# Kernel optimization log

Measured on AMD Instinct MI355X. Metric: run time of the kernel, lower is better.

The kernel has to match this reference:

```python
import jax, jax.numpy as jnp
import numpy as np

D_MODEL = 2048
NUM_HEADS = 32
HEAD_DIM = D_MODEL // NUM_HEADS  # 64
ROPE_BASE = 10000.0


def _rope_cos_sin(seq_len, head_dim, dtype):
    inv_freq = 1.0 / (ROPE_BASE ** (jnp.arange(0, head_dim, 2, dtype=jnp.float32) / head_dim))
    freqs = jnp.arange(seq_len, dtype=jnp.float32)[:, None] * inv_freq[None, :]  # (S, Dh/2)
    emb = jnp.concatenate([freqs, freqs], axis=-1)  # (S, Dh)
    return emb.astype(dtype), jnp.cos(emb).astype(dtype), jnp.sin(emb).astype(dtype)


def _rotate_half(x):
    x1, x2 = jnp.split(x, 2, axis=-1)
    return jnp.concatenate([-x2, x1], axis=-1)


def setup_inputs() -> dict:
    key = jax.random.key(0)
    k1, k2, k3, k4 = jax.random.split(key, 4)
    B, S, D = 1, 2048, D_MODEL
    x = jax.random.normal(k1, (B, S, D), dtype=jnp.float32)
    Wqkv = jax.random.normal(k2, (3 * D, D), dtype=jnp.float32) * 0.02
    Wo = jax.random.normal(k3, (D, D), dtype=jnp.float32) * 0.02
    gate = jax.random.normal(k4, (D,), dtype=jnp.float32) * 0.1
    return {"x": x, "Wqkv": Wqkv, "Wo": Wo, "gate": gate}


def reference(x, Wqkv, Wo, gate):
    B, S, D = x.shape
    H, Dh = NUM_HEADS, HEAD_DIM
    residual = x

    # fused QKV projection (torch Linear: y = x @ W.T)
    qkv = jnp.einsum('bsd,ed->bse', x, Wqkv).reshape(B, S, 3, H, Dh)
    q, k, v = qkv[:, :, 0], qkv[:, :, 1], qkv[:, :, 2]  # each (B, S, H, Dh)

    # RoPE
    _, cos, sin = _rope_cos_sin(S, Dh, x.dtype)
    cos = cos[None, :, None, :]  # (1, S, 1, Dh)
    sin = sin[None, :, None, :]
    q = q * cos + _rotate_half(q) * sin
    k = k * cos + _rotate_half(k) * sin

    # causal SDPA
    scale = 1.0 / np.sqrt(Dh)
    scores = jnp.einsum('bqhd,bkhd->bhqk', q, k) * scale  # (B, H, S, S)
    causal = jnp.tril(jnp.ones((S, S), dtype=bool))
    scores = jnp.where(causal[None, None], scores, jnp.finfo(scores.dtype).min)
    probs = jax.nn.softmax(scores, axis=-1)
    attn = jnp.einsum('bhqk,bkhd->bqhd', probs, v).reshape(B, S, D)

    out = jnp.einsum('bsd,ed->bse', attn, Wo)
    # HeoGate: learned per-channel gated residual (assumption; see notes)
    return residual + gate * out
```

## Files before the change

kernel.cpp:

```cpp
#include <hip/hip_runtime.h>
#include <hip/hip_bf16.h>
#include <cstdint>
#include <cstddef>

typedef __hip_bfloat16 bf16;
typedef short short8 __attribute__((ext_vector_type(8)));
typedef float f32x4 __attribute__((ext_vector_type(4)));

#define S_LEN 2048
#define DMODEL 2048
#define NQKV 6144
#define NHEADS 32
#define HDIM 64
#define ROPE_L2 0.4152410118609203f
#define Q_PRESCALE 0.18033688011112042f

__device__ __forceinline__ void async_copy16(const bf16* g, bf16* l) {
  __builtin_amdgcn_global_load_lds(
      (const __attribute__((address_space(1))) void*)g,
      (__attribute__((address_space(3))) void*)l, 16, 0, 0);
}

__device__ __forceinline__ f32x4 mfma_bf16(short8 a, short8 b, f32x4 c) {
  return __builtin_amdgcn_mfma_f32_16x16x32_bf16(a, b, c, 0, 0, 0);
}

__global__ __launch_bounds__(256) void cvt3_kernel(const float* __restrict__ sx,
                                                   bf16* __restrict__ dx,
                                                   const float* __restrict__ sw,
                                                   bf16* __restrict__ dw,
                                                   const float* __restrict__ so,
                                                   bf16* __restrict__ dov) {
  int i = blockIdx.x * 256 + threadIdx.x;
  const float* s;
  bf16* d;
  if (i < 1048576) {
    s = sx; d = dx;
  } else if (i < 4194304) {
    s = sw; d = dw; i -= 1048576;
  } else {
    s = so; d = dov; i -= 4194304;
  }
  const float4 v = ((const float4*)s)[i];
  union { bf16 h[4]; ushort4 u; } tmp;
  tmp.h[0] = __float2bfloat16(v.x);
  tmp.h[1] = __float2bfloat16(v.y);
  tmp.h[2] = __float2bfloat16(v.z);
  tmp.h[3] = __float2bfloat16(v.w);
  ((ushort4*)d)[i] = tmp.u;
}

#define QKV_NT 32
#define QBAR() do { __builtin_amdgcn_s_barrier(); __builtin_amdgcn_sched_barrier(0); } while (0)
#define WAITV(n) asm volatile("s_waitcnt vmcnt(" #n ")" ::: "memory")
#define LGKM0() do { asm volatile("s_waitcnt lgkmcnt(0)" ::: "memory"); \
                     __builtin_amdgcn_sched_barrier(0); } while (0)

__global__ __launch_bounds__(256, 2) void gemm_qkv(const bf16* __restrict__ A,
                                                   const bf16* __restrict__ W,
                                                   bf16* __restrict__ q_ws,
                                                   bf16* __restrict__ k_ws,
                                                   bf16* __restrict__ v_ws) {
  __shared__ bf16 smem[32768];
  const int tid = threadIdx.x;
  const int wave = tid >> 6, lane = tid & 63;
  const int wm = wave >> 1, wn = wave & 1;
  const int m0 = blockIdx.y * 128, n0 = blockIdx.x * 128;
  const int srow = tid >> 2;
  const int swc = (((tid & 3) ^ ((tid >> 3) & 3)) * 8);
  const int fr = lane & 15, fq = lane >> 4;
  const int rdc = ((fq ^ ((fr >> 1) & 3)) * 8);

  const bf16* Asrc = A + (size_t)(m0 + srow) * DMODEL + swc;
  const bf16* Bsrc = W + (size_t)(n0 + srow) * DMODEL + swc;

  auto stage = [&](int t_, int bufe_) {
#pragma unroll
    for (int kk = 0; kk < 2; ++kk) {
      const int ko = t_ * 64 + kk * 32;
      async_copy16(Asrc + ko, &smem[bufe_ + kk * 4096 + wave * 512]);
      async_copy16(Asrc + (size_t)64 * DMODEL + ko,
                   &smem[bufe_ + kk * 4096 + 2048 + wave * 512]);
      async_copy16(Bsrc + ko, &smem[bufe_ + 8192 + kk * 4096 + wave * 512]);
      async_copy16(Bsrc + (size_t)64 * DMODEL + ko,
                   &smem[bufe_ + 8192 + kk * 4096 + 2048 + wave * 512]);
    }
  };

  const f32x4 zero = {0.f, 0.f, 0.f, 0.f};
  f32x4 acc[4][4];
#pragma unroll
  for (int i = 0; i < 4; ++i)
#pragma unroll
    for (int j = 0; j < 4; ++j) acc[i][j] = zero;
  short8 a0[4], a1[4], b0[4], b1[4];

  stage(0, 0);
  stage(1, 16384);
  WAITV(8);
  QBAR();

#pragma unroll 2
  for (int t = 0; t < QKV_NT; ++t) {
    const int bc = (t & 1) * 16384;
#pragma unroll
    for (int mi = 0; mi < 4; ++mi) {
      const int ro = (wm * 64 + mi * 16 + fr) * 32 + rdc;
      a0[mi] = *(const short8*)&smem[bc + ro];
      a1[mi] = *(const short8*)&smem[bc + 4096 + ro];
    }
#pragma unroll
    for (int n = 0; n < 4; ++n) {
      const int ro = (wn * 64 + n * 16 + fr) * 32 + rdc;
      b0[n] = *(const short8*)&smem[bc + 8192 + ro];
      b1[n] = *(const short8*)&smem[bc + 12288 + ro];
    }
    LGKM0();
    QBAR();
    if (t + 2 < QKV_NT) stage(t + 2, bc);
    __builtin_amdgcn_s_setprio(1);
#pragma unroll
    for (int mi = 0; mi < 4; ++mi)
#pragma unroll
      for (int n = 0; n < 4; ++n)
        acc[mi][n] = mfma_bf16(a0[mi], b0[n], acc[mi][n]);
#pragma unroll
    for (int mi = 0; mi < 4; ++mi)
#pragma unroll
      for (int n = 0; n < 4; ++n)
        acc[mi][n] = mfma_bf16(a1[mi], b1[n], acc[mi][n]);
    __builtin_amdgcn_s_setprio(0);
    if (t + 2 < QKV_NT)      { WAITV(8); }
    else if (t + 1 < QKV_NT) { WAITV(0); }
    QBAR();
  }

  const int colb = n0 + wn * 64;
  const int sect = colb >> 11;
  const int h = (colb & 2047) >> 6;
  const int col = fr, rq = fq * 4;

  if (sect < 2) {
    bf16* dst = ((sect == 0) ? q_ws : k_ws) + (size_t)h * S_LEN * HDIM;
    bf16* rep = smem + wave * 1152;
    const float qs = (sect == 0) ? Q_PRESCALE : 1.0f;
    const float f0 = exp2f(-(float)col * ROPE_L2);
    const float f1 = exp2f(-(float)(16 + col) * ROPE_L2);
    __syncthreads();
    for (int m = 0; m < 4; ++m) {
      const int base_s = m0 + wm * 64 + m * 16;
#pragma unroll
      for (int jl = 0; jl < 2; ++jl) {
        const int dh = jl * 16 + col;
        const float fr_ = (jl == 0) ? f0 : f1;
#pragma unroll
        for (int r = 0; r < 4; ++r) {
          const int srw = base_s + rq + r;
          float sn, cs;
          __sincosf((float)srw * fr_, &sn, &cs);
          const float xl = acc[m][jl][r], xh = acc[m][jl + 2][r];
          rep[(rq + r) * 72 + dh]      = __float2bfloat16((xl * cs - xh * sn) * qs);
          rep[(rq + r) * 72 + dh + 32] = __float2bfloat16((xh * cs + xl * sn) * qs);
        }
      }
#pragma unroll
      for (int p = 0; p < 2; ++p) {
        const int rr = p * 8 + (lane >> 3), ch = lane & 7;
        const uint4 vv = *(const uint4*)&rep[rr * 72 + ch * 8];
        *(uint4*)&dst[(size_t)(base_s + rr) * HDIM + ch * 8] = vv;
      }
    }
  } else {
    bf16* dst = v_ws + (size_t)h * HDIM * S_LEN;
    for (int j = 0; j < 4; ++j) {
      const int dh = j * 16 + col;
      for (int m = 0; m < 4; ++m) {
        const int s0 = m0 + wm * 64 + m * 16 + rq;
        union { bf16 hx[4]; uint2 u; } vk;
#pragma unroll
        for (int r = 0; r < 4; ++r) vk.hx[r] = __float2bfloat16(acc[m][j][r]);
        *(uint2*)&dst[(size_t)dh * S_LEN + s0] = vk.u;
      }
    }
  }
}

__global__ __launch_bounds__(512) void attn_kernel(const bf16* __restrict__ q_ws,
                                                   const bf16* __restrict__ k_ws,
                                                   const bf16* __restrict__ vt_ws,
                                                   bf16* __restrict__ attn_out) {
  const int bid = blockIdx.x;
  const int qt = 15 - (bid >> 5);
  const int h = bid & 31;

  const int tid = threadIdx.x, wave = tid >> 6, lane = tid & 63;
  const int col = lane & 15, fq = lane >> 4;
  const int q_glob = qt * 128 + wave * 16 + col;

  __shared__ bf16 Ks[2][64 * 64];
  __shared__ bf16 Vs[2][64 * 64];
  __shared__ bf16 Pl[8][16 * 72];
  bf16* pl = Pl[wave];

  const bf16* qh = q_ws + (size_t)h * S_LEN * HDIM;
  const bf16* kh = k_ws + (size_t)h * S_LEN * HDIM;
  const bf16* vh = vt_ws + (size_t)h * HDIM * S_LEN;

  const int srow = lane >> 3;
  const int slot = lane & 7;
  const int schunk = slot ^ srow;

  auto stage = [&](int kt, int buf) {
    const int k0 = kt * 64;
    const int r8 = wave * 8;
    async_copy16(kh + (size_t)(k0 + r8 + srow) * HDIM + schunk * 8,
                 &Ks[buf][r8 * 64]);
    async_copy16(vh + (size_t)(r8 + srow) * S_LEN + k0 + schunk * 8,
                 &Vs[buf][r8 * 64]);
  };

  short8 qf[2];
#pragma unroll
  for (int ks = 0; ks < 2; ++ks)
    qf[ks] = *(const short8*)&qh[(size_t)q_glob * HDIM + ks * 32 + fq * 8];

  const f32x4 zero = {0.f, 0.f, 0.f, 0.f};
  f32x4 o_acc[4] = {zero, zero, zero, zero};
  float m_i = -1e30f, l_i = 0.f;

  stage(0, 0);

  const int lastk = 2 * qt + 1;
  for (int kt = 0; kt <= lastk; ++kt) {
    const int buf = kt & 1;
    const int k0 = kt * 64;
    __syncthreads();
    if (kt < lastk) stage(kt + 1, buf ^ 1);

    short8 kf[8];
#pragma unroll
    for (int n = 0; n < 4; ++n) {
      const int row = n * 16 + col;
#pragma unroll
      for (int ks = 0; ks < 2; ++ks)
        kf[n * 2 + ks] =
            *(const short8*)&Ks[buf][row * 64 + (((ks * 4 + fq) ^ (row & 7)) * 8)];
    }
    f32x4 s_acc[4] = {zero, zero, zero, zero};
#pragma unroll
    for (int n = 0; n < 4; ++n)
#pragma unroll
      for (int ks = 0; ks < 2; ++ks)
        s_acc[n] = mfma_bf16(kf[n * 2 + ks], qf[ks], s_acc[n]);

    short8 vf[8];
#pragma unroll
    for (int n = 0; n < 4; ++n) {
      const int row = n * 16 + col;
#pragma unroll
      for (int ks = 0; ks < 2; ++ks)
        vf[n * 2 + ks] =
            *(const short8*)&Vs[buf][row * 64 + (((ks * 4 + fq) ^ (row & 7)) * 8)];
    }

    if (k0 + 63 > qt * 128 + wave * 16) {
#pragma unroll
      for (int n = 0; n < 4; ++n)
#pragma unroll
        for (int r = 0; r < 4; ++r)
          if (k0 + n * 16 + fq * 4 + r > q_glob) s_acc[n][r] = -1e30f;
    }

    float vmax = -1e30f;
#pragma unroll
    for (int n = 0; n < 4; ++n)
#pragma unroll
      for (int r = 0; r < 4; ++r) vmax = fmaxf(vmax, s_acc[n][r]);
    vmax = fmaxf(vmax, __shfl_xor(vmax, 16, 64));
    vmax = fmaxf(vmax, __shfl_xor(vmax, 32, 64));

    if (!__all(vmax - m_i <= 8.0f)) {
      const float mnew = fmaxf(m_i, vmax);
      const float alpha = exp2f(m_i - mnew);
      l_i *= alpha;
#pragma unroll
      for (int n = 0; n < 4; ++n)
#pragma unroll
        for (int r = 0; r < 4; ++r) o_acc[n][r] *= alpha;
      m_i = mnew;
    }

    float rs = 0.f;
#pragma unroll
    for (int n = 0; n < 4; ++n)
#pragma unroll
      for (int r = 0; r < 4; ++r) {
        const float p = exp2f(s_acc[n][r] - m_i);
        s_acc[n][r] = p;
        rs += p;
      }
    rs += __shfl_xor(rs, 16, 64);
    rs += __shfl_xor(rs, 32, 64);
    l_i += rs;

#pragma unroll
    for (int n = 0; n < 4; ++n) {
      union { bf16 hx[4]; uint2 u; } pk;
#pragma unroll
      for (int r = 0; r < 4; ++r) pk.hx[r] = __float2bfloat16(s_acc[n][r]);
      *(uint2*)&pl[col * 72 + n * 16 + fq * 4] = pk.u;
    }
    short8 pa[2];
#pragma unroll
    for (int ks = 0; ks < 2; ++ks)
      pa[ks] = *(const short8*)&pl[col * 72 + ks * 32 + fq * 8];

#pragma unroll
    for (int n = 0; n < 4; ++n)
#pragma unroll
      for (int ks = 0; ks < 2; ++ks)
        o_acc[n] = mfma_bf16(vf[n * 2 + ks], pa[ks], o_acc[n]);
  }

  const float inv = 1.0f / l_i;
#pragma unroll
  for (int n = 0; n < 4; ++n) {
#pragma unroll
    for (int r = 0; r < 4; ++r) o_acc[n][r] *= inv;
    union { bf16 hx[4]; uint2 u; } ok;
#pragma unroll
    for (int r = 0; r < 4; ++r) ok.hx[r] = __float2bfloat16(o_acc[n][r]);
    *(uint2*)&attn_out[(size_t)q_glob * DMODEL + h * HDIM + n * 16 + fq * 4] = ok.u;
  }
}

__global__ __launch_bounds__(256, 2) void gemm_out(const bf16* __restrict__ A,
                                                   const bf16* __restrict__ W,
                                                   const float* __restrict__ xres,
                                                   const float* __restrict__ gate,
                                                   float* __restrict__ out) {
  constexpr int K = DMODEL;
  constexpr int NT = K / 64;
  __shared__ bf16 smem[2][12288];
  const int tid = threadIdx.x;
  const int wave = tid >> 6, lane = tid & 63;
  const int m0 = blockIdx.y * 64, n0 = blockIdx.x * 128;
  const int srow = tid >> 2;
  const int swc = (((tid & 3) ^ ((tid >> 3) & 3)) * 8);
  const int fr = lane & 15, fq = lane >> 4;
  const int rdc = ((fq ^ ((fr >> 1) & 3)) * 8);

  const bf16* Asrc = A + (size_t)(m0 + srow) * K + swc;
  const bf16* Bsrc = W + (size_t)(n0 + srow) * K + swc;

  auto stage = [&](int t_, int buf_) {
#pragma unroll
    for (int kk = 0; kk < 2; ++kk) {
      const int ko = t_ * 64 + kk * 32;
      async_copy16(Asrc + ko, &smem[buf_][kk * 2048 + wave * 512]);
      async_copy16(Bsrc + ko, &smem[buf_][4096 + kk * 4096 + wave * 512]);
      async_copy16(Bsrc + (size_t)64 * K + ko,
                   &smem[buf_][4096 + kk * 4096 + 2048 + wave * 512]);
    }
  };

  const f32x4 zero = {0.f, 0.f, 0.f, 0.f};
  f32x4 acc[4][2];
#pragma unroll
  for (int i = 0; i < 4; ++i)
#pragma unroll
    for (int j = 0; j < 2; ++j) acc[i][j] = zero;
  short8 a0[4], a1[4], b0[2], b1[2];

  stage(0, 0);
  stage(1, 1);
  WAITV(6);
  QBAR();

  for (int t = 0; t < NT; ++t) {
    const int bc = t & 1;
#pragma unroll
    for (int i = 0; i < 4; ++i) {
      const int ro = (i * 16 + fr) * 32 + rdc;
      a0[i] = *(const short8*)&smem[bc][ro];
      a1[i] = *(const short8*)&smem[bc][2048 + ro];
    }
#pragma unroll
    for (int j = 0; j < 2; ++j) {
      const int ro = (wave * 32 + j * 16 + fr) * 32 + rdc;
      b0[j] = *(const short8*)&smem[bc][4096 + ro];
      b1[j] = *(const short8*)&smem[bc][8192 + ro];
    }
    LGKM0();
    QBAR();
    if (t + 2 < NT) stage(t + 2, bc);
    __builtin_amdgcn_s_setprio(1);
#pragma unroll
    for (int i = 0; i < 4; ++i)
#pragma unroll
      for (int j = 0; j < 2; ++j)
        acc[i][j] = mfma_bf16(a0[i], b0[j], acc[i][j]);
#pragma unroll
    for (int i = 0; i < 4; ++i)
#pragma unroll
      for (int j = 0; j < 2; ++j)
        acc[i][j] = mfma_bf16(a1[i], b1[j], acc[i][j]);
    __builtin_amdgcn_s_setprio(0);
    if (t + 2 < NT)      { WAITV(6); }
    else if (t + 1 < NT) { WAITV(0); }
    QBAR();
  }

  const int col = fr, rq = fq * 4;
  for (int j = 0; j < 2; ++j) {
    const int cc = n0 + wave * 32 + j * 16 + col;
    const float g = gate[cc];
    for (int i = 0; i < 4; ++i) {
      const int base_row = m0 + i * 16 + rq;
      for (int r = 0; r < 4; ++r) {
        const size_t idx = (size_t)(base_row + r) * DMODEL + cc;
        out[idx] = xres[idx] + g * acc[i][j][r];
      }
    }
  }
}

extern "C" void kernel_launch(void* const* d_in, const int* in_sizes, int n_in,
                              void* d_out, int out_size, void* d_ws, size_t ws_size,
                              hipStream_t stream) {
  const float* x    = (const float*)d_in[0];
  const float* Wqkv = (const float*)d_in[1];
  const float* Wo   = (const float*)d_in[2];
  const float* gate = (const float*)d_in[3];
  float* out = (float*)d_out;

  char* ws = (char*)d_ws;
  const size_t MB = 1024 * 1024;
  bf16* xb      = (bf16*)(ws);
  bf16* wqkvb   = (bf16*)(ws + 8 * MB);
  bf16* wob     = (bf16*)(ws + 32 * MB);
  bf16* q_ws    = (bf16*)(ws + 40 * MB);
  bf16* k_ws    = (bf16*)(ws + 48 * MB);
  bf16* v_ws    = (bf16*)(ws + 56 * MB);
  bf16* attn_ws = (bf16*)(ws);

  cvt3_kernel<<<dim3(20480), 256, 0, stream>>>(x, xb, Wqkv, wqkvb, Wo, wob);

  gemm_qkv<<<dim3(NQKV / 128, S_LEN / 128), 256, 0, stream>>>(xb, wqkvb, q_ws, k_ws, v_ws);
  attn_kernel<<<dim3(512), 512, 0, stream>>>(q_ws, k_ws, v_ws, attn_ws);
  gemm_out<<<dim3(DMODEL / 128, DMODEL / 64), 256, 0, stream>>>(attn_ws, wob, x, gate, out);
}
```

Before: 248.2 us.

## Persistent tile loop for QKV GEMM and larger 128x128 tiles for output GEMM

The QKV projection GEMM now launches a fixed 512-block grid. Each block maps a linear tile index to its (m, n) tile, and the first 256 blocks process a second tile, so the 768 tiles are covered without a ragged extra launch wave. The output GEMM moves from 64x128 tiles with 4 waves to 128x128 tiles with 8 waves and 512 threads. This halves the block count and increases reuse of each loaded B panel, at the cost of more LDS and threads per block. The extra __syncthreads before reusing shared memory in the persistent loop adds some synchronisation overhead.

```diff
diff --git a/kernel.cpp b/kernel.cpp
--- a/kernel.cpp
+++ b/kernel.cpp
@@ -65,15 +65,15 @@
   const int tid = threadIdx.x;
   const int wave = tid >> 6, lane = tid & 63;
   const int wm = wave >> 1, wn = wave & 1;
-  const int m0 = blockIdx.y * 128, n0 = blockIdx.x * 128;
   const int srow = tid >> 2;
   const int swc = (((tid & 3) ^ ((tid >> 3) & 3)) * 8);
   const int fr = lane & 15, fq = lane >> 4;
   const int rdc = ((fq ^ ((fr >> 1) & 3)) * 8);
 
-  const bf16* Asrc = A + (size_t)(m0 + srow) * DMODEL + swc;
-  const bf16* Bsrc = W + (size_t)(n0 + srow) * DMODEL + swc;
-
+  const int b = blockIdx.x;
+  const int nrep = (b < 256) ? 2 : 1;
+
+  const bf16 *Asrc, *Bsrc;
   auto stage = [&](int t_, int bufe_) {
 #pragma unroll
     for (int kk = 0; kk < 2; ++kk) {
@@ -89,97 +89,107 @@
 
   const f32x4 zero = {0.f, 0.f, 0.f, 0.f};
   f32x4 acc[4][4];
-#pragma unroll
-  for (int i = 0; i < 4; ++i)
-#pragma unroll
-    for (int j = 0; j < 4; ++j) acc[i][j] = zero;
   short8 a0[4], a1[4], b0[4], b1[4];
 
-  stage(0, 0);
-  stage(1, 16384);
-  WAITV(8);
-  QBAR();
+  for (int rep = 0; rep < nrep; ++rep) {
+    const int tile = (rep == 0) ? b : (512 + b);
+    const int m0 = (tile / 48) * 128, n0 = (tile % 48) * 128;
+    Asrc = A + (size_t)(m0 + srow) * DMODEL + swc;
+    Bsrc = W + (size_t)(n0 + srow) * DMODEL + swc;
+
+#pragma unroll
+    for (int i = 0; i < 4; ++i)
+#pragma unroll
+      for (int j = 0; j < 4; ++j) acc[i][j] = zero;
+
+    if (rep) __syncthreads();
+
+    stage(0, 0);
+    stage(1, 16384);
+    WAITV(8);
+    QBAR();
 
 #pragma unroll 2
-  for (int t = 0; t < QKV_NT; ++t) {
-    const int bc = (t & 1) * 16384;
-#pragma unroll
-    for (int mi = 0; mi < 4; ++mi) {
-      const int ro = (wm * 64 + mi * 16 + fr) * 32 + rdc;
-      a0[mi] = *(const short8*)&smem[bc + ro];
-      a1[mi] = *(const short8*)&smem[bc + 4096 + ro];
-    }
-#pragma unroll
-    for (int n = 0; n < 4; ++n) {
-      const int ro = (wn * 64 + n * 16 + fr) * 32 + rdc;
-      b0[n] = *(const short8*)&smem[bc + 8192 + ro];
-      b1[n] = *(const short8*)&smem[bc + 12288 + ro];
-    }
-    LGKM0();
-    QBAR();
-    if (t + 2 < QKV_NT) stage(t + 2, bc);
-    __builtin_amdgcn_s_setprio(1);
-#pragma unroll
-    for (int mi = 0; mi < 4; ++mi)
-#pragma unroll
-      for (int n = 0; n < 4; ++n)
-        acc[mi][n] = mfma_bf16(a0[mi], b0[n], acc[mi][n]);
-#pragma unroll
-    for (int mi = 0; mi < 4; ++mi)
-#pragma unroll
-      for (int n = 0; n < 4; ++n)
-        acc[mi][n] = mfma_bf16(a1[mi], b1[n], acc[mi][n]);
-    __builtin_amdgcn_s_setprio(0);
-    if (t + 2 < QKV_NT)      { WAITV(8); }
-    else if (t + 1 < QKV_NT) { WAITV(0); }
-    QBAR();
-  }
-
-  const int colb = n0 + wn * 64;
-  const int sect = colb >> 11;
-  const int h = (colb & 2047) >> 6;
-  const int col = fr, rq = fq * 4;
-
-  if (sect < 2) {
-    bf16* dst = ((sect == 0) ? q_ws : k_ws) + (size_t)h * S_LEN * HDIM;
-    bf16* rep = smem + wave * 1152;
-    const float qs = (sect == 0) ? Q_PRESCALE : 1.0f;
-    const float f0 = exp2f(-(float)col * ROPE_L2);
-    const float f1 = exp2f(-(float)(16 + col) * ROPE_L2);
-    __syncthreads();
-    for (int m = 0; m < 4; ++m) {
-      const int base_s = m0 + wm * 64 + m * 16;
-#pragma unroll
-      for (int jl = 0; jl < 2; ++jl) {
-        const int dh = jl * 16 + col;
-        const float fr_ = (jl == 0) ? f0 : f1;
-#pragma unroll
-        for (int r = 0; r < 4; ++r) {
-          const int srw = base_s + rq + r;
-          float sn, cs;
-          __sincosf((float)srw * fr_, &sn, &cs);
-          const float xl = acc[m][jl][r], xh = acc[m][jl + 2][r];
-          rep[(rq + r) * 72 + dh]      = __float2bfloat16((xl * cs - xh * sn) * qs);
-          rep[(rq + r) * 72 + dh + 32] = __float2bfloat16((xh * cs + xl * sn) * qs);
+    for (int t = 0; t < QKV_NT; ++t) {
+      const int bc = (t & 1) * 16384;
+#pragma unroll
+      for (int mi = 0; mi < 4; ++mi) {
+        const int ro = (wm * 64 + mi * 16 + fr) * 32 + rdc;
+        a0[mi] = *(const short8*)&smem[bc + ro];
+        a1[mi] = *(const short8*)&smem[bc + 4096 + ro];
+      }
+#pragma unroll
+      for (int n = 0; n < 4; ++n) {
+        const int ro = (wn * 64 + n * 16 + fr) * 32 + rdc;
+        b0[n] = *(const short8*)&smem[bc + 8192 + ro];
+        b1[n] = *(const short8*)&smem[bc + 12288 + ro];
+      }
+      LGKM0();
+      QBAR();
+      if (t + 2 < QKV_NT) stage(t + 2, bc);
+      __builtin_amdgcn_s_setprio(1);
+#pragma unroll
+      for (int mi = 0; mi < 4; ++mi)
+#pragma unroll
+        for (int n = 0; n < 4; ++n)
+          acc[mi][n] = mfma_bf16(a0[mi], b0[n], acc[mi][n]);
+#pragma unroll
+      for (int mi = 0; mi < 4; ++mi)
+#pragma unroll
+        for (int n = 0; n < 4; ++n)
+          acc[mi][n] = mfma_bf16(a1[mi], b1[n], acc[mi][n]);
+      __builtin_amdgcn_s_setprio(0);
+      if (t + 2 < QKV_NT)      { WAITV(8); }
+      else if (t + 1 < QKV_NT) { WAITV(0); }
+      QBAR();
+    }
+
+    const int colb = n0 + wn * 64;
+    const int sect = colb >> 11;
+    const int h = (colb & 2047) >> 6;
+    const int col = fr, rq = fq * 4;
+
+    if (sect < 2) {
+      bf16* dst = ((sect == 0) ? q_ws : k_ws) + (size_t)h * S_LEN * HDIM;
+      bf16* rep_b = smem + wave * 1152;
+      const float qs = (sect == 0) ? Q_PRESCALE : 1.0f;
+      const float f0 = exp2f(-(float)col * ROPE_L2);
+      const float f1 = exp2f(-(float)(16 + col) * ROPE_L2);
+      __syncthreads();
+      for (int m = 0; m < 4; ++m) {
+        const int base_s = m0 + wm * 64 + m * 16;
+#pragma unroll
+        for (int jl = 0; jl < 2; ++jl) {
+          const int dh = jl * 16 + col;
+          const float fr_ = (jl == 0) ? f0 : f1;
+#pragma unroll
+          for (int r = 0; r < 4; ++r) {
+            const int srw = base_s + rq + r;
+            float sn, cs;
+            __sincosf((float)srw * fr_, &sn, &cs);
+            const float xl = acc[m][jl][r], xh = acc[m][jl + 2][r];
+            rep_b[(rq + r) * 72 + dh]      = __float2bfloat16((xl * cs - xh * sn) * qs);
+            rep_b[(rq + r) * 72 + dh + 32] = __float2bfloat16((xh * cs + xl * sn) * qs);
+          }
         }
-      }
-#pragma unroll
-      for (int p = 0; p < 2; ++p) {
-        const int rr = p * 8 + (lane >> 3), ch = lane & 7;
-        const uint4 vv = *(const uint4*)&rep[rr * 72 + ch * 8];
-        *(uint4*)&dst[(size_t)(base_s + rr) * HDIM + ch * 8] = vv;
-      }
-    }
-  } else {
-    bf16* dst = v_ws + (size_t)h * HDIM * S_LEN;
-    for (int j = 0; j < 4; ++j) {
-      const int dh = j * 16 + col;
-      for (int m = 0; m < 4; ++m) {
-        const int s0 = m0 + wm * 64 + m * 16 + rq;
-        union { bf16 hx[4]; uint2 u; } vk;
-#pragma unroll
-        for (int r = 0; r < 4; ++r) vk.hx[r] = __float2bfloat16(acc[m][j][r]);
-        *(uint2*)&dst[(size_t)dh * S_LEN + s0] = vk.u;
+#pragma unroll
+        for (int p = 0; p < 2; ++p) {
+          const int rr = p * 8 + (lane >> 3), ch = lane & 7;
+          const uint4 vv = *(const uint4*)&rep_b[rr * 72 + ch * 8];
+          *(uint4*)&dst[(size_t)(base_s + rr) * HDIM + ch * 8] = vv;
+        }
+      }
+    } else {
+      bf16* dst = v_ws + (size_t)h * HDIM * S_LEN;
+      for (int j = 0; j < 4; ++j) {
+        const int dh = j * 16 + col;
+        for (int m = 0; m < 4; ++m) {
+          const int s0 = m0 + wm * 64 + m * 16 + rq;
+          union { bf16 hx[4]; uint2 u; } vk;
+#pragma unroll
+          for (int r = 0; r < 4; ++r) vk.hx[r] = __float2bfloat16(acc[m][j][r]);
+          *(uint2*)&dst[(size_t)dh * S_LEN + s0] = vk.u;
+        }
       }
     }
   }
@@ -334,17 +344,18 @@
   }
 }
 
-__global__ __launch_bounds__(256, 2) void gemm_out(const bf16* __restrict__ A,
+__global__ __launch_bounds__(512, 2) void gemm_out(const bf16* __restrict__ A,
                                                    const bf16* __restrict__ W,
                                                    const float* __restrict__ xres,
                                                    const float* __restrict__ gate,
                                                    float* __restrict__ out) {
   constexpr int K = DMODEL;
   constexpr int NT = K / 64;
-  __shared__ bf16 smem[2][12288];
+  __shared__ bf16 smem[32768];
   const int tid = threadIdx.x;
   const int wave = tid >> 6, lane = tid & 63;
-  const int m0 = blockIdx.y * 64, n0 = blockIdx.x * 128;
+  const int wm = wave >> 2, wn = wave & 3;
+  const int m0 = blockIdx.y * 128, n0 = blockIdx.x * 128;
   const int srow = tid >> 2;
   const int swc = (((tid & 3) ^ ((tid >> 3) & 3)) * 8);
   const int fr = lane & 15, fq = lane >> 4;
@@ -353,14 +364,12 @@
   const bf16* Asrc = A + (size_t)(m0 + srow) * K + swc;
   const bf16* Bsrc = W + (size_t)(n0 + srow) * K + swc;
 
-  auto stage = [&](int t_, int buf_) {
+  auto stage = [&](int t_, int bufe_) {
 #pragma unroll
     for (int kk = 0; kk < 2; ++kk) {
       const int ko = t_ * 64 + kk * 32;
-      async_copy16(Asrc + ko, &smem[buf_][kk * 2048 + wave * 512]);
-      async_copy16(Bsrc + ko, &smem[buf_][4096 + kk * 4096 + wave * 512]);
-      async_copy16(Bsrc + (size_t)64 * K + ko,
-                   &smem[buf_][4096 + kk * 4096 + 2048 + wave * 512]);
+      async_copy16(Asrc + ko, &smem[bufe_ + kk * 4096 + wave * 512]);
+      async_copy16(Bsrc + ko, &smem[bufe_ + 8192 + kk * 4096 + wave * 512]);
     }
   };
 
@@ -373,23 +382,23 @@
   short8 a0[4], a1[4], b0[2], b1[2];
 
   stage(0, 0);
-  stage(1, 1);
-  WAITV(6);
+  stage(1, 16384);
+  WAITV(4);
   QBAR();
 
   for (int t = 0; t < NT; ++t) {
-    const int bc = t & 1;
+    const int bc = (t & 1) * 16384;
 #pragma unroll
     for (int i = 0; i < 4; ++i) {
-      const int ro = (i * 16 + fr) * 32 + rdc;
-      a0[i] = *(const short8*)&smem[bc][ro];
-      a1[i] = *(const short8*)&smem[bc][2048 + ro];
+      const int ro = (wm * 64 + i * 16 + fr) * 32 + rdc;
+      a0[i] = *(const short8*)&smem[bc + ro];
+      a1[i] = *(const short8*)&smem[bc + 4096 + ro];
     }
 #pragma unroll
     for (int j = 0; j < 2; ++j) {
-      const int ro = (wave * 32 + j * 16 + fr) * 32 + rdc;
-      b0[j] = *(const short8*)&smem[bc][4096 + ro];
-      b1[j] = *(const short8*)&smem[bc][8192 + ro];
+      const int ro = (wn * 32 + j * 16 + fr) * 32 + rdc;
+      b0[j] = *(const short8*)&smem[bc + 8192 + ro];
+      b1[j] = *(const short8*)&smem[bc + 12288 + ro];
     }
     LGKM0();
     QBAR();
@@ -406,17 +415,17 @@
       for (int j = 0; j < 2; ++j)
         acc[i][j] = mfma_bf16(a1[i], b1[j], acc[i][j]);
     __builtin_amdgcn_s_setprio(0);
-    if (t + 2 < NT)      { WAITV(6); }
+    if (t + 2 < NT)      { WAITV(4); }
     else if (t + 1 < NT) { WAITV(0); }
     QBAR();
   }
 
   const int col = fr, rq = fq * 4;
   for (int j = 0; j < 2; ++j) {
-    const int cc = n0 + wave * 32 + j * 16 + col;
+    const int cc = n0 + wn * 32 + j * 16 + col;
     const float g = gate[cc];
     for (int i = 0; i < 4; ++i) {
-      const int base_row = m0 + i * 16 + rq;
+      const int base_row = m0 + wm * 64 + i * 16 + rq;
       for (int r = 0; r < 4; ++r) {
         const size_t idx = (size_t)(base_row + r) * DMODEL + cc;
         out[idx] = xres[idx] + g * acc[i][j][r];
@@ -446,7 +455,7 @@
 
   cvt3_kernel<<<dim3(20480), 256, 0, stream>>>(x, xb, Wqkv, wqkvb, Wo, wob);
 
-  gemm_qkv<<<dim3(NQKV / 128, S_LEN / 128), 256, 0, stream>>>(xb, wqkvb, q_ws, k_ws, v_ws);
+  gemm_qkv<<<dim3(512), 256, 0, stream>>>(xb, wqkvb, q_ws, k_ws, v_ws);
   attn_kernel<<<dim3(512), 512, 0, stream>>>(q_ws, k_ws, v_ws, attn_ws);
-  gemm_out<<<dim3(DMODEL / 128, DMODEL / 64), 256, 0, stream>>>(attn_ws, wob, x, gate, out);
-}
+  gemm_out<<<dim3(DMODEL / 128, DMODEL / 128), 512, 0, stream>>>(attn_ws, wob, x, gate, out);
+}
```

Measured after the change: 247.4 us. No clear change (-0.3%).
